# Optimization experiments

Measured on AMD Instinct MI355X. Metric: run time of the kernel, lower is better.

Reference implementation:

```python
import jax, jax.numpy as jnp
import numpy as np

T, B, OBS, H, A = 512, 64, 512, 1024, 18


def setup_inputs() -> dict:
    key = jax.random.key(0)
    ks = jax.random.split(key, 8)
    s = lambda fan: 1.0 / np.sqrt(fan)
    return {
        "obs": jax.random.normal(ks[0], (T, B, OBS), jnp.float32),
        # binary done/valid mask per (timestep, env)
        "mask": (jax.random.uniform(ks[1], (T, B)) > 0.05).astype(jnp.float32),
        "W_enc": jax.random.normal(ks[2], (H, OBS), jnp.float32) * s(OBS),
        "b_enc": jnp.zeros((H,), jnp.float32),
        "W_ih": jax.random.normal(ks[3], (4 * H, H), jnp.float32) * s(H),
        "b_ih": jnp.zeros((4 * H,), jnp.float32),
        "W_hh": jax.random.normal(ks[4], (4 * H, H), jnp.float32) * s(H),
        "b_hh": jnp.zeros((4 * H,), jnp.float32),
        "W_dec": jax.random.normal(ks[5], (A, H), jnp.float32) * s(H),
        "b_dec": jnp.zeros((A,), jnp.float32),
    }


def reference(obs, mask, W_enc, b_enc, W_ih, b_ih, W_hh, b_hh, W_dec, b_dec):
    # encoder MLP + relu, batched over all T*B (one big GEMM)
    encoded = jax.nn.relu(jnp.einsum("tbo,ho->tbh", obs, W_enc) + b_enc)
    # precompute input contribution to LSTM gates for all timesteps: [T,B,4H]
    x_gates = jnp.einsum("tbh,gh->tbg", encoded, W_ih) + b_ih + b_hh

    def step(carry, inp):
        h, c = carry
        xg, m = inp  # xg: [B,4H], m: [B]
        gates = xg + h @ W_hh.T
        i, f, g, o = jnp.split(gates, 4, axis=-1)  # torch LSTMCell order
        c_new = jax.nn.sigmoid(f) * c + jax.nn.sigmoid(i) * jnp.tanh(g)
        h_new = jax.nn.sigmoid(o) * jnp.tanh(c_new)
        m = m[:, None]
        h_new = h_new * m
        c_new = c_new * m
        return (h_new, c_new), h_new

    h0 = jnp.zeros((B, H), jnp.float32)
    c0 = jnp.zeros((B, H), jnp.float32)
    (h, c), latent = jax.lax.scan(step, (h0, c0), (x_gates, mask))

    # decoder over flattened (T*B, H) then mask q-values
    values = jnp.einsum("tbh,ah->tba", latent, W_dec) + b_dec
    values = values * mask[..., None]
    return values, h, c
```

## Files before the change

kernel.cpp:

```cpp
#include <hip/hip_runtime.h>
#include <hip/hip_bf16.h>

#define T_ 512
#define B_ 64
#define OBS_ 512
#define H_ 1024
#define A_ 18
#define MM_ (T_*B_)
#define G4_ (4*H_)
#define CH_ 64
#define NCH_ (T_/CH_)
#define CM_ (CH_*B_)

typedef unsigned short u16;
typedef unsigned long long u64;
typedef __attribute__((ext_vector_type(8))) short s8v;
typedef __attribute__((ext_vector_type(4))) float f4v;

__device__ __forceinline__ float b2f(u16 u){
    unsigned x = ((unsigned)u) << 16;
    return __builtin_bit_cast(float, x);
}
__device__ __forceinline__ u16 f2b(float f){
    unsigned x = __builtin_bit_cast(unsigned, f);
    return (u16)((x + 0x7fffu + ((x >> 16) & 1u)) >> 16);
}


__global__ void cast_f32_bf16(const float* __restrict__ in, u16* __restrict__ out, int n){
    int i = blockIdx.x * blockDim.x + threadIdx.x;
    int stride = gridDim.x * blockDim.x;
    for (; i < n; i += stride) out[i] = f2b(in[i]);
}

__global__ void add_bias2(const float* __restrict__ a, const float* __restrict__ b,
                          float* __restrict__ out, int n){
    int i = blockIdx.x * blockDim.x + threadIdx.x;
    if (i < n) out[i] = a[i] + b[i];
}

__global__ void init_scan(u16* __restrict__ h_hist, float* __restrict__ c,
                          unsigned* __restrict__ flags){
    int i = blockIdx.x * blockDim.x + threadIdx.x;
    int stride = gridDim.x * blockDim.x;
    unsigned* h0 = (unsigned*)h_hist;
    for (int k = i; k < B_*H_/2; k += stride) h0[k] = 0u;
    for (int k = i; k < B_*H_; k += stride) c[k] = 0.f;
    if (i < 512) flags[i] = 0u;
}

__global__ void copy_hc(const float* __restrict__ h, const float* __restrict__ c,
                        float* __restrict__ out){
    int i = blockIdx.x * blockDim.x + threadIdx.x;
    out[(size_t)MM_*A_ + i] = h[i];
    out[(size_t)MM_*A_ + B_*H_ + i] = c[i];
}


#define LDSS 72

template<bool A_FP32, bool RELU>
__global__ __launch_bounds__(256) void gemm_bt(
    const void* __restrict__ Aptr, const u16* __restrict__ W,
    const float* __restrict__ bias, u16* __restrict__ C,
    int M, int N, int K)
{
    __shared__ __align__(16) u16 As[128 * LDSS];
    __shared__ __align__(16) u16 Bs[128 * LDSS];

    const int tid  = threadIdx.x;
    const int lane = tid & 63;
    const int wid  = tid >> 6;
    const int wm   = wid & 1, wn = wid >> 1;
    const int m0   = blockIdx.y * 128, n0 = blockIdx.x * 128;
    const int quad = lane >> 4, l16 = lane & 15;

    f4v acc[4][4];
    #pragma unroll
    for (int i = 0; i < 4; i++)
        #pragma unroll
        for (int j = 0; j < 4; j++) acc[i][j] = (f4v){0.f,0.f,0.f,0.f};

    for (int k0 = 0; k0 < K; k0 += 64){
        __syncthreads();
        if (A_FP32){
            const float* A = (const float*)Aptr;
            #pragma unroll
            for (int pss = 0; pss < 8; pss++){
                int idx = pss * 256 + tid;
                int row = idx >> 4, ch = idx & 15;
                float4 v = *(const float4*)(A + (size_t)(m0 + row) * K + k0 + ch * 4);
                u16* d = &As[row * LDSS + ch * 4];
                d[0] = f2b(v.x); d[1] = f2b(v.y); d[2] = f2b(v.z); d[3] = f2b(v.w);
            }
        } else {
            const u16* A = (const u16*)Aptr;
            #pragma unroll
            for (int pss = 0; pss < 4; pss++){
                int idx = pss * 256 + tid;
                int row = idx >> 3, ch = idx & 7;
                *(uint4*)&As[row * LDSS + ch * 8] =
                    *(const uint4*)(A + (size_t)(m0 + row) * K + k0 + ch * 8);
            }
        }
        #pragma unroll
        for (int pss = 0; pss < 4; pss++){
            int idx = pss * 256 + tid;
            int row = idx >> 3, ch = idx & 7;
            *(uint4*)&Bs[row * LDSS + ch * 8] =
                *(const uint4*)(W + (size_t)(n0 + row) * K + k0 + ch * 8);
        }
        __syncthreads();

        #pragma unroll
        for (int kk = 0; kk < 64; kk += 32){
            s8v af[4], bf[4];
            #pragma unroll
            for (int mt = 0; mt < 4; mt++)
                af[mt] = *(const s8v*)&As[(wm*64 + mt*16 + l16) * LDSS + kk + quad*8];
            #pragma unroll
            for (int nt = 0; nt < 4; nt++)
                bf[nt] = *(const s8v*)&Bs[(wn*64 + nt*16 + l16) * LDSS + kk + quad*8];
            #pragma unroll
            for (int mt = 0; mt < 4; mt++)
                #pragma unroll
                for (int nt = 0; nt < 4; nt++)
                    acc[mt][nt] = __builtin_amdgcn_mfma_f32_16x16x32_bf16(
                        af[mt], bf[nt], acc[mt][nt], 0, 0, 0);
        }
    }

    #pragma unroll
    for (int mt = 0; mt < 4; mt++){
        #pragma unroll
        for (int nt = 0; nt < 4; nt++){
            #pragma unroll
            for (int r = 0; r < 4; r++){
                int m = m0 + wm*64 + mt*16 + quad*4 + r;
                int n = n0 + wn*64 + nt*16 + l16;
                float v = acc[mt][nt][r] + bias[n];
                if (RELU) v = fmaxf(v, 0.f);
                C[(size_t)m * N + n] = f2b(v);
            }
        }
    }
}


__global__ __launch_bounds__(256, 1) void lstm_scan(
    const u16* __restrict__ xg,
    const u16* __restrict__ Whh,
    u16* __restrict__ h_hist,
    float* __restrict__ c_glob,
    float* __restrict__ h_f32,
    const float* __restrict__ mask,
    unsigned* __restrict__ flags,
    int t0)
{
    __shared__ float red[4][4][16][17];

    const int tid  = threadIdx.x;
    const int lane = tid & 63;
    const int w    = tid >> 6;
    const int quad = lane >> 4, l16 = lane & 15;
    const int bid  = blockIdx.x;
    const int g = bid & 3, s = bid >> 2;
    const int rb0 = g * 16, j0 = s * 16;

    const int koff = w * 256;
    s8v bf[4][8];
    #pragma unroll
    for (int gate = 0; gate < 4; gate++)
        #pragma unroll
        for (int ks = 0; ks < 8; ks++)
            bf[gate][ks] = *(const s8v*)(
                Whh + (size_t)(gate * H_ + j0 + l16) * H_ + koff + ks * 32 + quad * 8);

    const int cb = tid >> 4, cu = tid & 15;
    const size_t cidx = (size_t)(rb0 + cb) * H_ + j0 + cu;
    float c_reg = c_glob[cidx];

    const size_t hoff = (size_t)(rb0 + l16) * H_ + koff + quad * 8;

    unsigned* myflag = flags + ((g * 4 + (s >> 4)) << 5) + (s & 15);
    const unsigned* pollp = flags + ((g * 4 + w) << 5) + l16;

    const u16* xg0 = xg + (size_t)(rb0 + cb) * G4_ + j0 + cu;
    u16 nxi = xg0[0], nxf = xg0[H_], nxv = xg0[2 * H_], nxo = xg0[3 * H_];
    float nm = mask[rb0 + cb];

    for (int st = 0; st < CH_; st++){
        const float xi = b2f(nxi), xf = b2f(nxf), xv = b2f(nxv), xo = b2f(nxo);
        const float m = nm;

        const unsigned tgt = (unsigned)(t0 + st);
        int tries = 0;
        for (;;){
            unsigned f = __hip_atomic_load(pollp, __ATOMIC_RELAXED, __HIP_MEMORY_SCOPE_AGENT);
            if (__all((int)(f >= tgt))) break;
            if (++tries > (1 << 20)) break;
            if (tries >= 8) __builtin_amdgcn_s_sleep(1);
        }

        const u16* hs = h_hist + (size_t)st * B_ * H_ + hoff;
        f4v acc[4];
        #pragma unroll
        for (int gate = 0; gate < 4; gate++) acc[gate] = (f4v){0.f,0.f,0.f,0.f};
        #pragma unroll
        for (int ks = 0; ks < 8; ks++){
            s8v af = *(const s8v*)(hs + ks * 32);
            #pragma unroll
            for (int gate = 0; gate < 4; gate++)
                acc[gate] = __builtin_amdgcn_mfma_f32_16x16x32_bf16(af, bf[gate][ks], acc[gate], 0, 0, 0);
        }
        #pragma unroll
        for (int gate = 0; gate < 4; gate++)
            #pragma unroll
            for (int r = 0; r < 4; r++)
                red[w][gate][quad * 4 + r][l16] = acc[gate][r];
        __syncthreads();

        float gi = xi, gf = xf, gg = xv, go = xo;
        #pragma unroll
        for (int ww = 0; ww < 4; ww++){
            gi += red[ww][0][cb][cu];
            gf += red[ww][1][cb][cu];
            gg += red[ww][2][cb][cu];
            go += red[ww][3][cb][cu];
        }

        float is = 1.f / (1.f + __expf(-gi));
        float fs = 1.f / (1.f + __expf(-gf));
        float os = 1.f / (1.f + __expf(-go));
        float gt = tanhf(gg);

        float cn = fs * c_reg + is * gt;
        float hn = os * tanhf(cn);
        hn *= m; cn *= m;
        c_reg = cn;
        if (t0 + st == T_ - 1) h_f32[cidx] = hn;

        unsigned hb = (unsigned)f2b(hn);
        unsigned partner = (unsigned)__shfl_xor((int)hb, 1, 64);
        if ((cu & 1) == 0){
            unsigned packed = hb | (partner << 16);
            unsigned* dst = (unsigned*)(h_hist + (size_t)(st + 1) * B_ * H_ + cidx);
            __hip_atomic_store(dst, packed, __ATOMIC_RELAXED, __HIP_MEMORY_SCOPE_AGENT);
            if (st == CH_ - 1){
                unsigned* dst0 = (unsigned*)(h_hist + cidx);
                __hip_atomic_store(dst0, packed, __ATOMIC_RELAXED, __HIP_MEMORY_SCOPE_AGENT);
            }
        }
        asm volatile("s_waitcnt vmcnt(0)" ::: "memory");
        __syncthreads();

        if (tid == 0)
            __hip_atomic_store(myflag, (unsigned)(t0 + st + 1),
                               __ATOMIC_RELAXED, __HIP_MEMORY_SCOPE_AGENT);

        if (st + 1 < CH_){
            const u16* xgn = xg + (size_t)(st + 1) * B_ * G4_ + (size_t)(rb0 + cb) * G4_ + j0 + cu;
            nxi = xgn[0]; nxf = xgn[H_]; nxv = xgn[2 * H_]; nxo = xgn[3 * H_];
            nm = mask[(size_t)(st + 1) * B_ + rb0 + cb];
        }
    }

    c_glob[cidx] = c_reg;
}


__global__ __launch_bounds__(256) void decode_kernel(
    const u16* __restrict__ latent, const u16* __restrict__ Wdec,
    const float* __restrict__ bdec, const float* __restrict__ mask,
    float* __restrict__ values, int rows)
{
    __shared__ __align__(16) u16 wl[A_ * H_];
    const int tid = threadIdx.x;
    for (int i = tid; i < A_ * H_ / 8; i += 256)
        ((uint4*)wl)[i] = ((const uint4*)Wdec)[i];
    __syncthreads();

    const int lane = tid & 63;
    int wid = blockIdx.x * 4 + (tid >> 6);
    const int nwaves = gridDim.x * 4;

    for (int row = wid; row < rows; row += nwaves){
        float lat[16];
        #pragma unroll
        for (int i = 0; i < 16; i++)
            lat[i] = b2f(latent[(size_t)row * H_ + i*64 + lane]);
        float acc[A_];
        #pragma unroll
        for (int a = 0; a < A_; a++) acc[a] = 0.f;
        #pragma unroll
        for (int i = 0; i < 16; i++){
            #pragma unroll
            for (int a = 0; a < A_; a++)
                acc[a] += lat[i] * b2f(wl[a * H_ + i*64 + lane]);
        }
        float m = mask[row];
        #pragma unroll
        for (int a = 0; a < A_; a++){
            float v = acc[a];
            #pragma unroll
            for (int s = 32; s > 0; s >>= 1) v += __shfl_down(v, s, 64);
            if (lane == 0) values[(size_t)row * A_ + a] = (v + bdec[a]) * m;
        }
    }
}


extern "C" void kernel_launch(void* const* d_in, const int* in_sizes, int n_in,
                              void* d_out, int out_size, void* d_ws, size_t ws_size,
                              hipStream_t stream)
{
    const float* obs  = (const float*)d_in[0];
    const float* mask = (const float*)d_in[1];
    const float* Wenc = (const float*)d_in[2];
    const float* benc = (const float*)d_in[3];
    const float* Wih  = (const float*)d_in[4];
    const float* bih  = (const float*)d_in[5];
    const float* Whh  = (const float*)d_in[6];
    const float* bhh  = (const float*)d_in[7];
    const float* Wdec = (const float*)d_in[8];
    const float* bdec = (const float*)d_in[9];
    float* out = (float*)d_out;

    char* p = (char*)d_ws;
    size_t o = 0;
    auto alloc = [&](size_t bytes){ void* r = p + o; o += (bytes + 255) & ~(size_t)255; return r; };
    u16*      wenc_b  = (u16*)     alloc((size_t)H_ * OBS_ * 2);
    u16*      wih_b   = (u16*)     alloc((size_t)G4_ * H_ * 2);
    u16*      whh_b   = (u16*)     alloc((size_t)G4_ * H_ * 2);
    u16*      wdec_b  = (u16*)     alloc((size_t)A_ * H_ * 2);
    float*    bias2   = (float*)   alloc((size_t)G4_ * 4);
    u16*      enc_ch  = (u16*)     alloc((size_t)CM_ * H_ * 2);
    u16*      xg_ch   = (u16*)     alloc((size_t)CM_ * G4_ * 2);
    u16*      h_hist  = (u16*)     alloc((size_t)(CH_ + 1) * B_ * H_ * 2);
    float*    h_f32   = (float*)   alloc((size_t)B_ * H_ * 4);
    float*    c_f32   = (float*)   alloc((size_t)B_ * H_ * 4);
    unsigned* flags   = (unsigned*)alloc(512 * 4);
    (void)ws_size; (void)in_sizes; (void)n_in; (void)out_size;

    cast_f32_bf16<<<1024, 256, 0, stream>>>(Wenc, wenc_b, H_ * OBS_);
    cast_f32_bf16<<<2048, 256, 0, stream>>>(Wih,  wih_b,  G4_ * H_);
    cast_f32_bf16<<<2048, 256, 0, stream>>>(Whh,  whh_b,  G4_ * H_);
    cast_f32_bf16<<<72,   256, 0, stream>>>(Wdec, wdec_b, A_ * H_);
    add_bias2<<<16, 256, 0, stream>>>(bih, bhh, bias2, G4_);
    init_scan<<<2048, 256, 0, stream>>>(h_hist, c_f32, flags);

    for (int c = 0; c < NCH_; c++){
        const int t0 = c * CH_;

        dim3 g1(H_ / 128, CM_ / 128);
        gemm_bt<true, true><<<g1, 256, 0, stream>>>(
            obs + (size_t)t0 * B_ * OBS_, wenc_b, benc, enc_ch, CM_, H_, OBS_);

        dim3 g2(G4_ / 128, CM_ / 128);
        gemm_bt<false, false><<<g2, 256, 0, stream>>>(
            enc_ch, wih_b, bias2, xg_ch, CM_, G4_, H_);

        lstm_scan<<<256, 256, 0, stream>>>(
            xg_ch, whh_b, h_hist, c_f32, h_f32,
            mask + (size_t)t0 * B_, flags, t0);

        decode_kernel<<<256, 256, 0, stream>>>(
            h_hist + (size_t)B_ * H_, wdec_b, bdec, mask + (size_t)t0 * B_,
            out + (size_t)t0 * B_ * A_, CM_);
    }

    copy_hc<<<256, 256, 0, stream>>>(h_f32, c_f32, out);
}
```

Before: 2.630 ms.

## Use per-wave flags, fast activations, fused prep, and single encoder GEMM

Each wave now publishes its own progress flag and waits only on the flags it needs, instead of a block-wide barrier before tid 0 signals, so producers signal sooner. Sigmoid and tanh switch to rcp/exp approximations. The weight casts, bias add and state init are merged into one prep kernel. When the workspace is large enough, the encoder GEMM runs once over all timesteps instead of once per chunk. The cost is a larger flag array, more polling traffic, slightly less accurate activations and more workspace on the big path.

New measurement: 2.575 ms. -2.1%, faster.

```diff
diff --git a/kernel.cpp b/kernel.cpp
--- a/kernel.cpp
+++ b/kernel.cpp
@@ -26,27 +26,35 @@
     return (u16)((x + 0x7fffu + ((x >> 16) & 1u)) >> 16);
 }
 
-
-__global__ void cast_f32_bf16(const float* __restrict__ in, u16* __restrict__ out, int n){
+__device__ __forceinline__ float fsig(float x){
+    return __builtin_amdgcn_rcpf(1.f + __expf(-x));
+}
+__device__ __forceinline__ float ftanh(float x){
+    return 1.f - 2.f * __builtin_amdgcn_rcpf(__expf(2.f * x) + 1.f);
+}
+
+
+__global__ void prep_all(const float* __restrict__ Wenc, const float* __restrict__ Wih,
+                         const float* __restrict__ Whh, const float* __restrict__ Wdec,
+                         const float* __restrict__ bih, const float* __restrict__ bhh,
+                         u16* __restrict__ wenc_b, u16* __restrict__ wih_b,
+                         u16* __restrict__ whh_b, u16* __restrict__ wdec_b,
+                         float* __restrict__ bias2, u16* __restrict__ h_hist,
+                         float* __restrict__ c_f32, unsigned* __restrict__ flags)
+{
     int i = blockIdx.x * blockDim.x + threadIdx.x;
     int stride = gridDim.x * blockDim.x;
-    for (; i < n; i += stride) out[i] = f2b(in[i]);
-}
-
-__global__ void add_bias2(const float* __restrict__ a, const float* __restrict__ b,
-                          float* __restrict__ out, int n){
-    int i = blockIdx.x * blockDim.x + threadIdx.x;
-    if (i < n) out[i] = a[i] + b[i];
-}
-
-__global__ void init_scan(u16* __restrict__ h_hist, float* __restrict__ c,
-                          unsigned* __restrict__ flags){
-    int i = blockIdx.x * blockDim.x + threadIdx.x;
-    int stride = gridDim.x * blockDim.x;
+    for (int k = i; k < G4_ * H_; k += stride){
+        wih_b[k] = f2b(Wih[k]);
+        whh_b[k] = f2b(Whh[k]);
+    }
+    for (int k = i; k < H_ * OBS_; k += stride) wenc_b[k] = f2b(Wenc[k]);
+    for (int k = i; k < A_ * H_; k += stride) wdec_b[k] = f2b(Wdec[k]);
+    for (int k = i; k < G4_; k += stride) bias2[k] = bih[k] + bhh[k];
     unsigned* h0 = (unsigned*)h_hist;
-    for (int k = i; k < B_*H_/2; k += stride) h0[k] = 0u;
-    for (int k = i; k < B_*H_; k += stride) c[k] = 0.f;
-    if (i < 512) flags[i] = 0u;
+    for (int k = i; k < B_ * H_ / 2; k += stride) h0[k] = 0u;
+    for (int k = i; k < B_ * H_; k += stride) c_f32[k] = 0.f;
+    for (int k = i; k < 1024; k += stride) flags[k] = 0u;
 }
 
 __global__ void copy_hc(const float* __restrict__ h, const float* __restrict__ c,
@@ -182,8 +190,8 @@
 
     const size_t hoff = (size_t)(rb0 + l16) * H_ + koff + quad * 8;
 
-    unsigned* myflag = flags + ((g * 4 + (s >> 4)) << 5) + (s & 15);
-    const unsigned* pollp = flags + ((g * 4 + w) << 5) + l16;
+    unsigned* myflag = flags + (g << 8) + (s << 2) + w;
+    const unsigned* pollp = flags + (g << 8) + (w << 6) + lane;
 
     const u16* xg0 = xg + (size_t)(rb0 + cb) * G4_ + j0 + cu;
     u16 nxi = xg0[0], nxf = xg0[H_], nxv = xg0[2 * H_], nxo = xg0[3 * H_];
@@ -229,13 +237,13 @@
             go += red[ww][3][cb][cu];
         }
 
-        float is = 1.f / (1.f + __expf(-gi));
-        float fs = 1.f / (1.f + __expf(-gf));
-        float os = 1.f / (1.f + __expf(-go));
-        float gt = tanhf(gg);
+        float is = fsig(gi);
+        float fs = fsig(gf);
+        float os = fsig(go);
+        float gt = ftanh(gg);
 
         float cn = fs * c_reg + is * gt;
-        float hn = os * tanhf(cn);
+        float hn = os * ftanh(cn);
         hn *= m; cn *= m;
         c_reg = cn;
         if (t0 + st == T_ - 1) h_f32[cidx] = hn;
@@ -252,9 +260,8 @@
             }
         }
         asm volatile("s_waitcnt vmcnt(0)" ::: "memory");
-        __syncthreads();
-
-        if (tid == 0)
+
+        if (lane == 0)
             __hip_atomic_store(myflag, (unsigned)(t0 + st + 1),
                                __ATOMIC_RELAXED, __HIP_MEMORY_SCOPE_AGENT);
 
@@ -263,6 +270,8 @@
             nxi = xgn[0]; nxf = xgn[H_]; nxv = xgn[2 * H_]; nxo = xgn[3 * H_];
             nm = mask[(size_t)(st + 1) * B_ + rb0 + cb];
         }
+
+        __syncthreads();
     }
 
     c_glob[cidx] = c_reg;
@@ -334,39 +343,64 @@
     u16*      whh_b   = (u16*)     alloc((size_t)G4_ * H_ * 2);
     u16*      wdec_b  = (u16*)     alloc((size_t)A_ * H_ * 2);
     float*    bias2   = (float*)   alloc((size_t)G4_ * 4);
-    u16*      enc_ch  = (u16*)     alloc((size_t)CM_ * H_ * 2);
-    u16*      xg_ch   = (u16*)     alloc((size_t)CM_ * G4_ * 2);
     u16*      h_hist  = (u16*)     alloc((size_t)(CH_ + 1) * B_ * H_ * 2);
     float*    h_f32   = (float*)   alloc((size_t)B_ * H_ * 4);
     float*    c_f32   = (float*)   alloc((size_t)B_ * H_ * 4);
-    unsigned* flags   = (unsigned*)alloc(512 * 4);
-    (void)ws_size; (void)in_sizes; (void)n_in; (void)out_size;
-
-    cast_f32_bf16<<<1024, 256, 0, stream>>>(Wenc, wenc_b, H_ * OBS_);
-    cast_f32_bf16<<<2048, 256, 0, stream>>>(Wih,  wih_b,  G4_ * H_);
-    cast_f32_bf16<<<2048, 256, 0, stream>>>(Whh,  whh_b,  G4_ * H_);
-    cast_f32_bf16<<<72,   256, 0, stream>>>(Wdec, wdec_b, A_ * H_);
-    add_bias2<<<16, 256, 0, stream>>>(bih, bhh, bias2, G4_);
-    init_scan<<<2048, 256, 0, stream>>>(h_hist, c_f32, flags);
-
-    for (int c = 0; c < NCH_; c++){
-        const int t0 = c * CH_;
-
-        dim3 g1(H_ / 128, CM_ / 128);
-        gemm_bt<true, true><<<g1, 256, 0, stream>>>(
-            obs + (size_t)t0 * B_ * OBS_, wenc_b, benc, enc_ch, CM_, H_, OBS_);
-
-        dim3 g2(G4_ / 128, CM_ / 128);
-        gemm_bt<false, false><<<g2, 256, 0, stream>>>(
-            enc_ch, wih_b, bias2, xg_ch, CM_, G4_, H_);
-
-        lstm_scan<<<256, 256, 0, stream>>>(
-            xg_ch, whh_b, h_hist, c_f32, h_f32,
-            mask + (size_t)t0 * B_, flags, t0);
-
-        decode_kernel<<<256, 256, 0, stream>>>(
-            h_hist + (size_t)B_ * H_, wdec_b, bdec, mask + (size_t)t0 * B_,
-            out + (size_t)t0 * B_ * A_, CM_);
+    unsigned* flags   = (unsigned*)alloc(1024 * 4);
+    u16*      xg_ch   = (u16*)     alloc((size_t)CM_ * G4_ * 2);
+
+    const size_t enc_all_b = (size_t)MM_ * H_ * 2;
+    const bool big = ws_size >= o + enc_all_b + 4096;
+    (void)in_sizes; (void)n_in; (void)out_size;
+
+    prep_all<<<2048, 256, 0, stream>>>(Wenc, Wih, Whh, Wdec, bih, bhh,
+                                       wenc_b, wih_b, whh_b, wdec_b,
+                                       bias2, h_hist, c_f32, flags);
+
+    if (big){
+        u16* enc_all = (u16*)alloc(enc_all_b);
+
+        dim3 ge(H_ / 128, MM_ / 128);
+        gemm_bt<true, true><<<ge, 256, 0, stream>>>(
+            obs, wenc_b, benc, enc_all, MM_, H_, OBS_);
+
+        for (int c = 0; c < NCH_; c++){
+            const int t0 = c * CH_;
+
+            dim3 gx(G4_ / 128, CM_ / 128);
+            gemm_bt<false, false><<<gx, 256, 0, stream>>>(
+                enc_all + (size_t)c * CM_ * H_, wih_b, bias2, xg_ch, CM_, G4_, H_);
+
+            lstm_scan<<<256, 256, 0, stream>>>(
+                xg_ch, whh_b, h_hist, c_f32, h_f32,
+                mask + (size_t)t0 * B_, flags, t0);
+
+            decode_kernel<<<256, 256, 0, stream>>>(
+                h_hist + (size_t)B_ * H_, wdec_b, bdec, mask + (size_t)t0 * B_,
+                out + (size_t)t0 * B_ * A_, CM_);
+        }
+    } else {
+        u16* enc_ch = (u16*)alloc((size_t)CM_ * H_ * 2);
+
+        for (int c = 0; c < NCH_; c++){
+            const int t0 = c * CH_;
+
+            dim3 g1(H_ / 128, CM_ / 128);
+            gemm_bt<true, true><<<g1, 256, 0, stream>>>(
+                obs + (size_t)t0 * B_ * OBS_, wenc_b, benc, enc_ch, CM_, H_, OBS_);
+
+            dim3 g2(G4_ / 128, CM_ / 128);
+            gemm_bt<false, false><<<g2, 256, 0, stream>>>(
+                enc_ch, wih_b, bias2, xg_ch, CM_, G4_, H_);
+
+            lstm_scan<<<256, 256, 0, stream>>>(
+                xg_ch, whh_b, h_hist, c_f32, h_f32,
+                mask + (size_t)t0 * B_, flags, t0);
+
+            decode_kernel<<<256, 256, 0, stream>>>(
+                h_hist + (size_t)B_ * H_, wdec_b, bdec, mask + (size_t)t0 * B_,
+                out + (size_t)t0 * B_ * A_, CM_);
+        }
     }
 
     copy_hc<<<256, 256, 0, stream>>>(h_f32, c_f32, out);
```
